# Performance work log

Hardware: AMD Instinct MI355X
Metric: run time of the kernel (lower is better)

The kernel has to match this reference:

```python
import jax, jax.numpy as jnp
import numpy as np


def _rbf_forward(batches, centers, beta, W, b):
    # Pairwise Euclidean distances via GEMM expansion instead of materializing
    # the O(n*K*dim) difference tensor the torch code builds.
    x2 = jnp.sum(batches * batches, axis=1, keepdims=True)          # [n, 1]
    c2 = jnp.sum(centers * centers, axis=1)                          # [K]
    xc = jnp.einsum('nd,kd->nk', batches, centers)                   # [n, K]
    d2 = jnp.maximum(x2 + c2[None, :] - 2.0 * xc, 0.0)               # [n, K]
    dist = jnp.sqrt(d2)
    radial = jnp.exp(-beta * dist)                                   # beta: [1, K]
    return radial @ W.T + b                                          # [n, num_class]


def setup_inputs() -> dict:
    key = jax.random.key(0)
    k1, k2, k3, k4, k5 = jax.random.split(key, 5)
    n, K, dim, num_class = 16384, 2048, 512, 10
    batches = jax.random.normal(k1, (n, dim), dtype=jnp.float32)
    centers = jax.random.normal(k2, (K, dim), dtype=jnp.float32)
    beta = jnp.full((1, K), 0.1, dtype=jnp.float32)  # torch init: ones/10
    W = jax.random.normal(k4, (num_class, K), dtype=jnp.float32) / np.sqrt(K)
    b = jax.random.normal(k5, (num_class,), dtype=jnp.float32) * 0.01
    return {"batches": batches, "centers": centers, "beta": beta, "W": W, "b": b}


def reference(batches, centers, beta, W, b):
    return _rbf_forward(batches, centers, beta, W, b)
```

## Files before the change

kernel.cpp:

```cpp
#include <hip/hip_runtime.h>
#include <hip/hip_bf16.h>
#include <stdint.h>

#define M_N  16384
#define K_C  2048
#define DIM  512
#define NCLS 10
#define NBN  (K_C / 128)

typedef unsigned short u16;
typedef float  f32x4  __attribute__((ext_vector_type(4)));
typedef __bf16 bf16x8 __attribute__((ext_vector_type(8)));


__device__ __forceinline__ void async_ld16(const void* g, void* l) {
  __builtin_amdgcn_global_load_lds(
      (const __attribute__((address_space(1))) void*)g,
      (__attribute__((address_space(3))) void*)l,
      16, 0, 0);
}

__device__ __forceinline__ u16 f2bf_rne(float f) {
  uint32_t u = __float_as_uint(f);
  u += 0x7FFFu + ((u >> 16) & 1u);
  return (u16)(u >> 16);
}


__global__ void convert_rows(const float4* __restrict__ src,
                             ushort4* __restrict__ dst,
                             float* __restrict__ sq) {
  int row = blockIdx.x;
  int t = threadIdx.x;
  float4 v = src[(size_t)row * 128 + t];
  float ss = v.x * v.x + v.y * v.y + v.z * v.z + v.w * v.w;
  ushort4 o;
  o.x = f2bf_rne(v.x); o.y = f2bf_rne(v.y);
  o.z = f2bf_rne(v.z); o.w = f2bf_rne(v.w);
  dst[(size_t)row * 128 + t] = o;
  ss += __shfl_down(ss, 32);
  ss += __shfl_down(ss, 16);
  ss += __shfl_down(ss, 8);
  ss += __shfl_down(ss, 4);
  ss += __shfl_down(ss, 2);
  ss += __shfl_down(ss, 1);
  __shared__ float part[2];
  if ((t & 63) == 0) part[t >> 6] = ss;
  __syncthreads();
  if (t == 0) sq[row] = part[0] + part[1];
}


__global__ void convert_w(const float* __restrict__ W, u16* __restrict__ Wbf) {
  int idx = blockIdx.x * 256 + threadIdx.x;
  int n = idx >> 11, k = idx & 2047;
  float v = (n < NCLS) ? W[n * K_C + k] : 0.0f;
  Wbf[idx] = f2bf_rne(v);
}


__global__ __launch_bounds__(256, 4) void rbf_main(
    const u16* __restrict__ A,
    const u16* __restrict__ B,
    const float* __restrict__ x2,
    const float* __restrict__ c2,
    const float* __restrict__ beta,
    const u16* __restrict__ Wbf,
    float* __restrict__ partial) {
  constexpr int BK = 64;
  __shared__ alignas(16) unsigned char smem[32768];
  u16* As = (u16*)smem;
  u16* Bs = (u16*)(smem + 16384);
  u16* Rt = (u16*)smem;

  const int tid  = threadIdx.x;
  const int lane = tid & 63;
  const int wid  = tid >> 6;
  const int bn = blockIdx.x, bm = blockIdx.y;
  const int row0 = bm * 128, col0 = bn * 128;
  const int wrC = (wid >> 1) * 64;
  const int wcB = (wid & 1) * 64;

  f32x4 acc[4][4] = {};

  const int srow = tid >> 3;
  const int scol = ((tid & 7) ^ (srow & 7)) * 8;
  const u16* aG = A + (size_t)(row0 + srow) * DIM + scol;
  const u16* bG = B + (size_t)(col0 + srow) * DIM + scol;
  u16* aL = As + tid * 8;
  u16* bL = Bs + tid * 8;

  const int frow = lane & 15;
  const int fq   = lane >> 4;
  const int fsw  = frow & 7;

  for (int k0 = 0; k0 < DIM; k0 += BK) {
    __syncthreads();
#pragma unroll
    for (int i = 0; i < 4; ++i) {
      async_ld16(aG + k0 + i * 32 * DIM, aL + i * 2048);
      async_ld16(bG + k0 + i * 32 * DIM, bL + i * 2048);
    }
    __syncthreads();

#pragma unroll
    for (int kh = 0; kh < 2; ++kh) {
      const int slot = ((kh << 2) | fq) ^ fsw;
      bf16x8 cf[4], bfr[4];
#pragma unroll
      for (int mi = 0; mi < 4; ++mi)
        cf[mi] = *(const bf16x8*)(Bs + (wrC + mi * 16 + frow) * BK + slot * 8);
#pragma unroll
      for (int ni = 0; ni < 4; ++ni)
        bfr[ni] = *(const bf16x8*)(As + (wcB + ni * 16 + frow) * BK + slot * 8);
#pragma unroll
      for (int mi = 0; mi < 4; ++mi)
#pragma unroll
        for (int ni = 0; ni < 4; ++ni)
          acc[mi][ni] = __builtin_amdgcn_mfma_f32_16x16x32_bf16(
              cf[mi], bfr[ni], acc[mi][ni], 0, 0, 0);
    }
  }

  const int cls = lane & 15, q = lane >> 4;
  bf16x8 wfr[4];
#pragma unroll
  for (int t = 0; t < 4; ++t)
    wfr[t] = *(const bf16x8*)(Wbf + (size_t)cls * K_C + col0 + t * 32 + q * 8);

  float4 c2q[4], btq[4];
#pragma unroll
  for (int mi = 0; mi < 4; ++mi) {
    int base = col0 + wrC + mi * 16 + q * 4;
    c2q[mi] = *(const float4*)(c2 + base);
    btq[mi] = *(const float4*)(beta + base);
  }
  float x2v[4];
#pragma unroll
  for (int ni = 0; ni < 4; ++ni)
    x2v[ni] = x2[row0 + wcB + ni * 16 + cls];

  __syncthreads();

  union Pack { u16 h[4]; uint2 v; };
#pragma unroll
  for (int mi = 0; mi < 4; ++mi) {
#pragma unroll
    for (int ni = 0; ni < 4; ++ni) {
      Pack pk;
#pragma unroll
      for (int r = 0; r < 4; ++r) {
        float xc = acc[mi][ni][r];
        float d2 = fmaxf(x2v[ni] + c2q[mi][r] - 2.0f * xc, 0.0f);
        float radial = __expf(-btq[mi][r] * sqrtf(d2));
        pk.h[r] = f2bf_rne(radial);
      }
      int br  = wcB + ni * 16 + cls;
      int cc0 = wrC + mi * 16 + q * 4;
      *(uint2*)(Rt + br * 128 + (cc0 ^ ((br & 15) << 3))) = pk.v;
    }
  }
  __syncthreads();

  f32x4 acc2[2] = {};
#pragma unroll
  for (int s2 = 0; s2 < 2; ++s2) {
    const int br = (wid * 2 + s2) * 16 + cls;
    const u16* rrow = Rt + br * 128;
    const int sw = cls << 3;
#pragma unroll
    for (int t = 0; t < 4; ++t) {
      bf16x8 ra = *(const bf16x8*)(rrow + ((t * 32 + q * 8) ^ sw));
      acc2[s2] = __builtin_amdgcn_mfma_f32_16x16x32_bf16(
          ra, wfr[t], acc2[s2], 0, 0, 0);
    }
  }

#pragma unroll
  for (int s2 = 0; s2 < 2; ++s2)
#pragma unroll
    for (int r = 0; r < 4; ++r) {
      int gr = row0 + (wid * 2 + s2) * 16 + q * 4 + r;
      partial[(size_t)gr * (NBN * 16) + bn * 16 + cls] = acc2[s2][r];
    }
}


__global__ void reduce_out(const float* __restrict__ partial,
                           const float* __restrict__ b,
                           float* __restrict__ out) {
  int idx = blockIdx.x * 256 + threadIdx.x;
  if (idx >= M_N * NCLS) return;
  int i = idx / NCLS, j = idx - i * NCLS;
  float s = b[j];
  const float* p = partial + (size_t)i * (NBN * 16) + j;
#pragma unroll
  for (int bn = 0; bn < NBN; ++bn) s += p[bn * 16];
  out[idx] = s;
}


extern "C" void kernel_launch(void* const* d_in, const int* in_sizes, int n_in,
                              void* d_out, int out_size, void* d_ws, size_t ws_size,
                              hipStream_t stream) {
  const float* batches = (const float*)d_in[0];
  const float* centers = (const float*)d_in[1];
  const float* beta    = (const float*)d_in[2];
  const float* W       = (const float*)d_in[3];
  const float* bias    = (const float*)d_in[4];
  float* out = (float*)d_out;

  char* ws = (char*)d_ws;
  u16*  Abf = (u16*)ws;
  u16*  Bbf = (u16*)(ws + (size_t)M_N * DIM * 2);
  float* x2 = (float*)(ws + (size_t)(M_N + K_C) * DIM * 2);
  float* c2 = x2 + M_N;
  u16*  Wbf = (u16*)(c2 + K_C);
  float* partial = (float*)((char*)Wbf + 16 * K_C * 2);

  convert_rows<<<dim3(M_N), dim3(128), 0, stream>>>(
      (const float4*)batches, (ushort4*)Abf, x2);
  convert_rows<<<dim3(K_C), dim3(128), 0, stream>>>(
      (const float4*)centers, (ushort4*)Bbf, c2);
  convert_w<<<dim3(16 * K_C / 256), dim3(256), 0, stream>>>(W, Wbf);
  rbf_main<<<dim3(NBN, M_N / 128), dim3(256), 0, stream>>>(
      Abf, Bbf, x2, c2, beta, Wbf, partial);
  reduce_out<<<dim3((M_N * NCLS + 255) / 256), dim3(256), 0, stream>>>(
      partial, bias, out);
}
```

Measured before the change: 147.8 us.

## Fuse preprocessing kernels, remap block order, and compact partial-sum layout

```diff
diff --git a/kernel.cpp b/kernel.cpp
--- a/kernel.cpp
+++ b/kernel.cpp
@@ -27,11 +27,10 @@
 }
 
 
-__global__ void convert_rows(const float4* __restrict__ src,
-                             ushort4* __restrict__ dst,
-                             float* __restrict__ sq) {
-  int row = blockIdx.x;
-  int t = threadIdx.x;
+__device__ __forceinline__ void conv_row(const float4* __restrict__ src,
+                                         ushort4* __restrict__ dst,
+                                         float* __restrict__ sq,
+                                         int row, int t) {
   float4 v = src[(size_t)row * 128 + t];
   float ss = v.x * v.x + v.y * v.y + v.z * v.z + v.w * v.w;
   ushort4 o;
@@ -50,12 +49,26 @@
   if (t == 0) sq[row] = part[0] + part[1];
 }
 
-
-__global__ void convert_w(const float* __restrict__ W, u16* __restrict__ Wbf) {
-  int idx = blockIdx.x * 256 + threadIdx.x;
-  int n = idx >> 11, k = idx & 2047;
-  float v = (n < NCLS) ? W[n * K_C + k] : 0.0f;
-  Wbf[idx] = f2bf_rne(v);
+__global__ void prep(const float4* __restrict__ batches,
+                     const float4* __restrict__ centers,
+                     const float* __restrict__ W,
+                     ushort4* __restrict__ Abf, ushort4* __restrict__ Bbf,
+                     float* __restrict__ x2, float* __restrict__ c2,
+                     u16* __restrict__ Wbf) {
+  int b = blockIdx.x, t = threadIdx.x;
+  if (b < M_N) {
+    conv_row(batches, Abf, x2, b, t);
+  } else if (b < M_N + K_C) {
+    conv_row(centers, Bbf, c2, b - M_N, t);
+  } else {
+    int wb = b - (M_N + K_C);
+#pragma unroll
+    for (int i = 0; i < 2; ++i) {
+      int idx = wb * 256 + i * 128 + t;
+      int n = idx >> 11, k = idx & 2047;
+      Wbf[idx] = (n < NCLS) ? f2bf_rne(W[n * K_C + k]) : (u16)0;
+    }
+  }
 }
 
 
@@ -76,7 +89,10 @@
   const int tid  = threadIdx.x;
   const int lane = tid & 63;
   const int wid  = tid >> 6;
-  const int bn = blockIdx.x, bm = blockIdx.y;
+  const int bid = blockIdx.x;
+  const int g = bid >> 3, r8 = bid & 7;
+  const int bm = r8 * 16 + (g & 15);
+  const int bn = g >> 4;
   const int row0 = bm * 128, col0 = bn * 128;
   const int wrC = (wid >> 1) * 64;
   const int wcB = (wid & 1) * 64;
@@ -123,11 +139,6 @@
   }
 
   const int cls = lane & 15, q = lane >> 4;
-  bf16x8 wfr[4];
-#pragma unroll
-  for (int t = 0; t < 4; ++t)
-    wfr[t] = *(const bf16x8*)(Wbf + (size_t)cls * K_C + col0 + t * 32 + q * 8);
-
   float4 c2q[4], btq[4];
 #pragma unroll
   for (int mi = 0; mi < 4; ++mi) {
@@ -162,6 +173,11 @@
   }
   __syncthreads();
 
+  bf16x8 wfr[4];
+#pragma unroll
+  for (int t = 0; t < 4; ++t)
+    wfr[t] = *(const bf16x8*)(Wbf + (size_t)cls * K_C + col0 + t * 32 + q * 8);
+
   f32x4 acc2[2] = {};
 #pragma unroll
   for (int s2 = 0; s2 < 2; ++s2) {
@@ -176,13 +192,16 @@
     }
   }
 
-#pragma unroll
-  for (int s2 = 0; s2 < 2; ++s2)
-#pragma unroll
-    for (int r = 0; r < 4; ++r) {
-      int gr = row0 + (wid * 2 + s2) * 16 + q * 4 + r;
-      partial[(size_t)gr * (NBN * 16) + bn * 16 + cls] = acc2[s2][r];
-    }
+  if (cls < NCLS) {
+#pragma unroll
+    for (int s2 = 0; s2 < 2; ++s2)
+#pragma unroll
+      for (int r = 0; r < 4; ++r) {
+        int gr = row0 + (wid * 2 + s2) * 16 + q * 4 + r;
+        partial[(size_t)bn * (M_N * NCLS) + (size_t)gr * NCLS + cls] =
+            acc2[s2][r];
+      }
+  }
 }
 
 
@@ -191,11 +210,11 @@
                            float* __restrict__ out) {
   int idx = blockIdx.x * 256 + threadIdx.x;
   if (idx >= M_N * NCLS) return;
-  int i = idx / NCLS, j = idx - i * NCLS;
+  int j = idx % NCLS;
   float s = b[j];
-  const float* p = partial + (size_t)i * (NBN * 16) + j;
-#pragma unroll
-  for (int bn = 0; bn < NBN; ++bn) s += p[bn * 16];
+#pragma unroll
+  for (int bn = 0; bn < NBN; ++bn)
+    s += partial[(size_t)bn * (M_N * NCLS) + idx];
   out[idx] = s;
 }
 
@@ -218,12 +237,10 @@
   u16*  Wbf = (u16*)(c2 + K_C);
   float* partial = (float*)((char*)Wbf + 16 * K_C * 2);
 
-  convert_rows<<<dim3(M_N), dim3(128), 0, stream>>>(
-      (const float4*)batches, (ushort4*)Abf, x2);
-  convert_rows<<<dim3(K_C), dim3(128), 0, stream>>>(
-      (const float4*)centers, (ushort4*)Bbf, c2);
-  convert_w<<<dim3(16 * K_C / 256), dim3(256), 0, stream>>>(W, Wbf);
-  rbf_main<<<dim3(NBN, M_N / 128), dim3(256), 0, stream>>>(
+  prep<<<dim3(M_N + K_C + 128), dim3(128), 0, stream>>>(
+      (const float4*)batches, (const float4*)centers, W,
+      (ushort4*)Abf, (ushort4*)Bbf, x2, c2, Wbf);
+  rbf_main<<<dim3(NBN * (M_N / 128)), dim3(256), 0, stream>>>(
       Abf, Bbf, x2, c2, beta, Wbf, partial);
   reduce_out<<<dim3((M_N * NCLS + 255) / 256), dim3(256), 0, stream>>>(
       partial, bias, out);
```

Measured after the change: 152.0 us. 2.9% more time.
